# Kernel tuning notes

Measured on AMD Instinct MI355X. Metric: run time of the kernel, lower is better.

Reference implementation:

```python
import jax, jax.numpy as jnp
import numpy as np

B = 1024

def _back_mask(mask_out, selh, selw, s, k, hin, win):
    # Mark which input positions (of this conv) are touched by sampled k x k patches.
    hc, wc = hin - k + 1, win - k + 1
    m = np.zeros((hin, win), np.float32)
    ho, wo = mask_out.shape
    for i in range(ho):
        for j in range(wo):
            if mask_out[i, j] > 0:
                ph = min(i * s + int(selh[i, j]), hc - 1)
                pw = min(j * s + int(selw[i, j]), wc - 1)
                m[ph:ph + k, pw:pw + k] = 1.0
    return m


def setup_inputs() -> dict:
    key = jax.random.key(0)
    ks = jax.random.split(key, 10)
    rng = np.random.default_rng(1)
    # stochastic pooling offsets, top-down as in the torch forward
    selh3 = rng.integers(0, 4, (1, 1)).astype(np.int32)
    selw3 = rng.integers(0, 4, (1, 1)).astype(np.int32)
    mask3 = np.ones((1, 1), np.float32)
    mask2 = _back_mask(mask3, selh3, selw3, s=4, k=3, hin=6, win=6)
    selh2 = rng.integers(0, 2, (6, 6)).astype(np.int32)
    selw2 = rng.integers(0, 2, (6, 6)).astype(np.int32)
    mask1 = _back_mask(mask2, selh2, selw2, s=2, k=3, hin=14, win=14)
    selh1 = rng.integers(0, 2, (14, 14)).astype(np.int32)
    selw1 = rng.integers(0, 2, (14, 14)).astype(np.int32)
    sc = 0.05
    return {
        "x": jax.random.normal(ks[0], (B, 3, 32, 32), jnp.float32),
        "W1": jax.random.normal(ks[1], (200, 3, 5, 5), jnp.float32) * sc,
        "b1": jax.random.normal(ks[2], (200,), jnp.float32) * sc,
        "W2": jax.random.normal(ks[3], (400, 200, 3, 3), jnp.float32) * sc,
        "b2": jax.random.normal(ks[4], (400,), jnp.float32) * sc,
        "W3": jax.random.normal(ks[5], (800, 400, 3, 3), jnp.float32) * sc,
        "b3": jax.random.normal(ks[6], (800,), jnp.float32) * sc,
        "fc_w": jax.random.normal(ks[7], (10, 800), jnp.float32) * sc,
        "fc_b": jax.random.normal(ks[8], (10,), jnp.float32) * sc,
        "selh1": jnp.asarray(selh1), "selw1": jnp.asarray(selw1),
        "selh2": jnp.asarray(selh2), "selw2": jnp.asarray(selw2),
        "selh3": jnp.asarray(selh3), "selw3": jnp.asarray(selw3),
        "mask1": jnp.asarray(mask1), "mask2": jnp.asarray(mask2),
        "mask3": jnp.asarray(mask3),
    }


def _sconv_avg(x, W, b, selh, selw, mask, k, s):
    # Stochastic conv+avgpool: compute stride-1 conv only at one sampled location
    # per pooling window, zero at masked-out output positions.
    Bq, C, H, Wd = x.shape
    hc, wc = H - k + 1, Wd - k + 1
    ho, wo = selh.shape
    ph = jnp.minimum(jnp.arange(ho)[:, None] * s + selh, hc - 1)  # (ho,wo)
    pw = jnp.minimum(jnp.arange(wo)[None, :] * s + selw, wc - 1)
    rows = ph[:, :, :, None] if False else (ph[..., None] + jnp.arange(k))  # (ho,wo,k)
    cols = pw[..., None] + jnp.arange(k)                                    # (ho,wo,k)
    # gather sampled k x k patches -> (B,C,ho,wo,k,k)
    patch = x[:, :, rows[:, :, :, None], cols[:, :, None, :]]
    out = jnp.einsum('bcxyij,ocij->boxy', patch, W) + b[None, :, None, None]
    return out * mask[None, None, :, :]


def reference(x, W1, b1, W2, b2, W3, b3, fc_w, fc_b,
              selh1, selw1, selh2, selw2, selh3, selw3,
              mask1, mask2, mask3):
    h = jax.nn.relu(_sconv_avg(x, W1, b1, selh1, selw1, mask1, k=5, s=2))   # (B,200,14,14)
    h = jax.nn.relu(_sconv_avg(h, W2, b2, selh2, selw2, mask2, k=3, s=2))   # (B,400,6,6)
    h = jax.nn.relu(_sconv_avg(h, W3, b3, selh3, selw3, mask3, k=3, s=4))   # (B,800,1,1)
    h = h.reshape(h.shape[0], -1)                                           # (B,800)
    return h @ fc_w.T + fc_b
```

## Files before the change

kernel.cpp:

```cpp
#include <hip/hip_runtime.h>


#define H1B_OFF 0ULL
#define P2_OFF  80281600ULL
#define W2B_OFF 114491392ULL
#define P3_OFF  116154368ULL
#define W3B_OFF 123625472ULL
#define H3_OFF  129695744ULL
#define W1T_OFF 132972544ULL

typedef unsigned short u16;
typedef short bf16x8 __attribute__((ext_vector_type(8)));
typedef float f32x4 __attribute__((ext_vector_type(4)));

__device__ __forceinline__ u16 f2bf(float f) {
    union { float f; unsigned int u; } v; v.f = f;
    unsigned int u = v.u + 0x7FFFu + ((v.u >> 16) & 1u);
    return (u16)(u >> 16);
}

__global__ __launch_bounds__(256) void wprep(
    const float* __restrict__ W1, const float* __restrict__ W2, const float* __restrict__ W3,
    float* __restrict__ W1t, u16* __restrict__ W2b, u16* __restrict__ W3b)
{
    int idx = blockIdx.x * 256 + threadIdx.x;
    if (idx < 16000) {
        int kk = idx / 200, oc = idx % 200;
        W1t[idx] = (kk < 75) ? W1[oc * 75 + kk] : 0.0f;
    } else if (idx < 16000 + 831488) {
        int j = idx - 16000;
        int oc = j / 1856, kk = j % 1856;
        float v = 0.0f;
        if (oc < 400 && kk < 1800) {
            int k3 = kk / 200, c = kk % 200;
            v = W2[oc * 1800 + c * 9 + k3];
        }
        W2b[j] = f2bf(v);
    } else if (idx < 16000 + 831488 + 3035136) {
        int j = idx - 16000 - 831488;
        int oc = j / 3648, kk = j % 3648;
        float v = 0.0f;
        if (oc < 800 && kk < 3600) {
            int k3 = kk / 400, c = kk % 400;
            v = W3[oc * 3600 + c * 9 + k3];
        }
        W3b[j] = f2bf(v);
    }
}

__global__ __launch_bounds__(256) void l1_kernel(
    const float* __restrict__ x, const float* __restrict__ W1t, const float* __restrict__ b1,
    const int* __restrict__ selh, const int* __restrict__ selw, const float* __restrict__ mask,
    u16* __restrict__ h1b)
{
    const int pos = blockIdx.x;
    const float m = mask[pos];
    if (m == 0.0f) return;
    const int i = pos / 14, j = pos % 14;
    const int b0 = blockIdx.y * 8;
    const int tid = threadIdx.x;
    const int ph = min(i * 2 + selh[pos], 27);
    const int pw = min(j * 2 + selw[pos], 27);

    __shared__ __align__(16) float sm[8 * 80];
    for (int e = tid; e < 640; e += 256) {
        int u = e / 80, kk = e % 80;
        float v = 0.0f;
        if (kk < 75) {
            int c = kk / 25, d = kk % 25;
            v = x[((b0 + u) * 3 + c) * 1024 + (ph + d / 5) * 32 + (pw + d % 5)];
        }
        sm[e] = v;
    }
    __syncthreads();
    if (tid < 200) {
        const int oc = tid;
        float bias = b1[oc];
        float acc[8];
#pragma unroll
        for (int u = 0; u < 8; ++u) acc[u] = bias;
        const float4* sm4 = reinterpret_cast<const float4*>(sm);
        for (int q = 0; q < 20; ++q) {
            float w0 = W1t[(q * 4 + 0) * 200 + oc];
            float w1 = W1t[(q * 4 + 1) * 200 + oc];
            float w2 = W1t[(q * 4 + 2) * 200 + oc];
            float w3 = W1t[(q * 4 + 3) * 200 + oc];
#pragma unroll
            for (int u = 0; u < 8; ++u) {
                float4 p = sm4[u * 20 + q];
                acc[u] = fmaf(w0, p.x, acc[u]);
                acc[u] = fmaf(w1, p.y, acc[u]);
                acc[u] = fmaf(w2, p.z, acc[u]);
                acc[u] = fmaf(w3, p.w, acc[u]);
            }
        }
#pragma unroll
        for (int u = 0; u < 8; ++u)
            h1b[((b0 + u) * 196 + pos) * 200 + oc] = f2bf(fmaxf(acc[u] * m, 0.0f));
    }
}

__global__ __launch_bounds__(256) void im2col2(
    const u16* __restrict__ h1b, const int* __restrict__ selh2, const int* __restrict__ selw2,
    const int* __restrict__ selh3, const int* __restrict__ selw3, u16* __restrict__ P2)
{
    int idx = blockIdx.x * 256 + threadIdx.x;
    int row = idx / 232, ch = idx % 232;
    if (row >= 9216) return;
    int b = row / 9, pidx = row % 9;
    int ph2 = min(selh3[0], 3), pw2 = min(selw3[0], 3);
    int pos = (ph2 + pidx / 3) * 6 + (pw2 + pidx % 3);
    int i = pos / 6, j = pos % 6;
    int ph = min(2 * i + selh2[pos], 11);
    int pw = min(2 * j + selw2[pos], 11);
    uint4 v = {0u, 0u, 0u, 0u};
    if (ch < 225) {
        int k3 = ch / 25, c8 = ch % 25;
        int srow = b * 196 + (ph + k3 / 3) * 14 + (pw + k3 % 3);
        v = *reinterpret_cast<const uint4*>(h1b + srow * 200 + c8 * 8);
    }
    *reinterpret_cast<uint4*>(P2 + (size_t)row * 1856 + ch * 8) = v;
}

__global__ __launch_bounds__(256) void padzero3(u16* __restrict__ P3)
{
    int idx = blockIdx.x * 256 + threadIdx.x;
    if (idx >= 6144) return;
    int b = idx / 6, c = idx % 6;
    uint4 z = {0u, 0u, 0u, 0u};
    *reinterpret_cast<uint4*>(P3 + (size_t)b * 3648 + 3600 + c * 8) = z;
}

__global__ __launch_bounds__(256) void gemm_l2(
    const u16* __restrict__ A, const u16* __restrict__ B,
    const float* __restrict__ bias, u16* __restrict__ P3)
{
    const int KP = 1856, NKT = 29;
    const int m0 = blockIdx.x * 64, n0 = blockIdx.y * 64;
    const int tid = threadIdx.x;
    const int lane = tid & 63, wid = tid >> 6;
    const int wm = wid >> 1, wn = wid & 1;

    __shared__ u16 Asm[64][72];
    __shared__ u16 Bsm[64][72];

    f32x4 zero = {0.f, 0.f, 0.f, 0.f};
    f32x4 acc00 = zero, acc01 = zero, acc10 = zero, acc11 = zero;

    const int ar = tid >> 3, ac = tid & 7;
    const uint4* Ag0 = reinterpret_cast<const uint4*>(A + (size_t)(m0 + ar) * KP + ac * 8);
    const uint4* Ag1 = reinterpret_cast<const uint4*>(A + (size_t)(m0 + ar + 32) * KP + ac * 8);
    const uint4* Bg0 = reinterpret_cast<const uint4*>(B + (size_t)(n0 + ar) * KP + ac * 8);
    const uint4* Bg1 = reinterpret_cast<const uint4*>(B + (size_t)(n0 + ar + 32) * KP + ac * 8);
    uint4* As0 = reinterpret_cast<uint4*>(&Asm[ar][ac * 8]);
    uint4* As1 = reinterpret_cast<uint4*>(&Asm[ar + 32][ac * 8]);
    uint4* Bs0 = reinterpret_cast<uint4*>(&Bsm[ar][ac * 8]);
    uint4* Bs1 = reinterpret_cast<uint4*>(&Bsm[ar + 32][ac * 8]);

    uint4 ra0 = Ag0[0], ra1 = Ag1[0], rb0 = Bg0[0], rb1 = Bg1[0];
    const int r = lane & 15, ks = lane >> 4;
    for (int kt = 0; kt < NKT; ++kt) {
        __syncthreads();
        *As0 = ra0; *As1 = ra1; *Bs0 = rb0; *Bs1 = rb1;
        __syncthreads();
        if (kt + 1 < NKT) {
            ra0 = Ag0[(kt + 1) * 8]; ra1 = Ag1[(kt + 1) * 8];
            rb0 = Bg0[(kt + 1) * 8]; rb1 = Bg1[(kt + 1) * 8];
        }
#pragma unroll
        for (int s = 0; s < 2; ++s) {
            bf16x8 a0 = *reinterpret_cast<const bf16x8*>(&Asm[wm * 32 + r][s * 32 + ks * 8]);
            bf16x8 a1 = *reinterpret_cast<const bf16x8*>(&Asm[wm * 32 + 16 + r][s * 32 + ks * 8]);
            bf16x8 b0 = *reinterpret_cast<const bf16x8*>(&Bsm[wn * 32 + r][s * 32 + ks * 8]);
            bf16x8 b1 = *reinterpret_cast<const bf16x8*>(&Bsm[wn * 32 + 16 + r][s * 32 + ks * 8]);
            acc00 = __builtin_amdgcn_mfma_f32_16x16x32_bf16(a0, b0, acc00, 0, 0, 0);
            acc01 = __builtin_amdgcn_mfma_f32_16x16x32_bf16(a0, b1, acc01, 0, 0, 0);
            acc10 = __builtin_amdgcn_mfma_f32_16x16x32_bf16(a1, b0, acc10, 0, 0, 0);
            acc11 = __builtin_amdgcn_mfma_f32_16x16x32_bf16(a1, b1, acc11, 0, 0, 0);
        }
    }
    const int colb = n0 + wn * 32 + (lane & 15);
    const int rowb = m0 + wm * 32 + ((lane >> 4) << 2);
#define L2STORE(ACC, MR, NR) { \
    int oc = colb + (NR) * 16; \
    if (oc < 400) { float bv = bias[oc]; \
        _Pragma("unroll") \
        for (int rr = 0; rr < 4; ++rr) { \
            int row = rowb + (MR) * 16 + rr; \
            int bq = row / 9, pq = row % 9; \
            P3[(size_t)bq * 3648 + pq * 400 + oc] = f2bf(fmaxf(ACC[rr] + bv, 0.0f)); \
        } } }
    L2STORE(acc00, 0, 0) L2STORE(acc01, 0, 1) L2STORE(acc10, 1, 0) L2STORE(acc11, 1, 1)
#undef L2STORE
}

__global__ __launch_bounds__(256) void gemm_l3(
    const u16* __restrict__ A, const u16* __restrict__ B,
    const float* __restrict__ bias, float* __restrict__ h3)
{
    const int KP = 3648, NKT = 57;
    const int m0 = blockIdx.x * 64, n0 = blockIdx.y * 64;
    const int tid = threadIdx.x;
    const int lane = tid & 63, wid = tid >> 6;
    const int wm = wid >> 1, wn = wid & 1;

    __shared__ u16 Asm[64][72];
    __shared__ u16 Bsm[64][72];

    f32x4 zero = {0.f, 0.f, 0.f, 0.f};
    f32x4 acc00 = zero, acc01 = zero, acc10 = zero, acc11 = zero;

    const int ar = tid >> 3, ac = tid & 7;
    const uint4* Ag0 = reinterpret_cast<const uint4*>(A + (size_t)(m0 + ar) * KP + ac * 8);
    const uint4* Ag1 = reinterpret_cast<const uint4*>(A + (size_t)(m0 + ar + 32) * KP + ac * 8);
    const uint4* Bg0 = reinterpret_cast<const uint4*>(B + (size_t)(n0 + ar) * KP + ac * 8);
    const uint4* Bg1 = reinterpret_cast<const uint4*>(B + (size_t)(n0 + ar + 32) * KP + ac * 8);
    uint4* As0 = reinterpret_cast<uint4*>(&Asm[ar][ac * 8]);
    uint4* As1 = reinterpret_cast<uint4*>(&Asm[ar + 32][ac * 8]);
    uint4* Bs0 = reinterpret_cast<uint4*>(&Bsm[ar][ac * 8]);
    uint4* Bs1 = reinterpret_cast<uint4*>(&Bsm[ar + 32][ac * 8]);

    uint4 ra0 = Ag0[0], ra1 = Ag1[0], rb0 = Bg0[0], rb1 = Bg1[0];
    const int r = lane & 15, ks = lane >> 4;
    for (int kt = 0; kt < NKT; ++kt) {
        __syncthreads();
        *As0 = ra0; *As1 = ra1; *Bs0 = rb0; *Bs1 = rb1;
        __syncthreads();
        if (kt + 1 < NKT) {
            ra0 = Ag0[(kt + 1) * 8]; ra1 = Ag1[(kt + 1) * 8];
            rb0 = Bg0[(kt + 1) * 8]; rb1 = Bg1[(kt + 1) * 8];
        }
#pragma unroll
        for (int s = 0; s < 2; ++s) {
            bf16x8 a0 = *reinterpret_cast<const bf16x8*>(&Asm[wm * 32 + r][s * 32 + ks * 8]);
            bf16x8 a1 = *reinterpret_cast<const bf16x8*>(&Asm[wm * 32 + 16 + r][s * 32 + ks * 8]);
            bf16x8 b0 = *reinterpret_cast<const bf16x8*>(&Bsm[wn * 32 + r][s * 32 + ks * 8]);
            bf16x8 b1 = *reinterpret_cast<const bf16x8*>(&Bsm[wn * 32 + 16 + r][s * 32 + ks * 8]);
            acc00 = __builtin_amdgcn_mfma_f32_16x16x32_bf16(a0, b0, acc00, 0, 0, 0);
            acc01 = __builtin_amdgcn_mfma_f32_16x16x32_bf16(a0, b1, acc01, 0, 0, 0);
            acc10 = __builtin_amdgcn_mfma_f32_16x16x32_bf16(a1, b0, acc10, 0, 0, 0);
            acc11 = __builtin_amdgcn_mfma_f32_16x16x32_bf16(a1, b1, acc11, 0, 0, 0);
        }
    }
    const int colb = n0 + wn * 32 + (lane & 15);
    const int rowb = m0 + wm * 32 + ((lane >> 4) << 2);
#define L3STORE(ACC, MR, NR) { \
    int oc = colb + (NR) * 16; \
    if (oc < 800) { float bv = bias[oc]; \
        _Pragma("unroll") \
        for (int rr = 0; rr < 4; ++rr) { \
            int row = rowb + (MR) * 16 + rr; \
            h3[(size_t)row * 800 + oc] = fmaxf(ACC[rr] + bv, 0.0f); \
        } } }
    L3STORE(acc00, 0, 0) L3STORE(acc01, 0, 1) L3STORE(acc10, 1, 0) L3STORE(acc11, 1, 1)
#undef L3STORE
}

__global__ __launch_bounds__(256) void fc_kernel(
    const float* __restrict__ h3, const float* __restrict__ fcw, const float* __restrict__ fcb,
    float* __restrict__ out)
{
    const int idx = blockIdx.x * 256 + threadIdx.x;
    if (idx >= 1024 * 10) return;
    const int b = idx / 10, o = idx % 10;
    float acc = fcb[o];
    const float4* hp = reinterpret_cast<const float4*>(h3 + b * 800);
    const float4* wp = reinterpret_cast<const float4*>(fcw + o * 800);
    for (int k = 0; k < 200; ++k) {
        float4 h = hp[k], w = wp[k];
        acc = fmaf(h.x, w.x, acc);
        acc = fmaf(h.y, w.y, acc);
        acc = fmaf(h.z, w.z, acc);
        acc = fmaf(h.w, w.w, acc);
    }
    out[idx] = acc;
}

extern "C" void kernel_launch(void* const* d_in, const int* in_sizes, int n_in,
                              void* d_out, int out_size, void* d_ws, size_t ws_size,
                              hipStream_t stream) {
    const float* x     = (const float*)d_in[0];
    const float* W1    = (const float*)d_in[1];
    const float* b1    = (const float*)d_in[2];
    const float* W2    = (const float*)d_in[3];
    const float* b2    = (const float*)d_in[4];
    const float* W3    = (const float*)d_in[5];
    const float* b3    = (const float*)d_in[6];
    const float* fc_w  = (const float*)d_in[7];
    const float* fc_b  = (const float*)d_in[8];
    const int*   selh1 = (const int*)d_in[9];
    const int*   selw1 = (const int*)d_in[10];
    const int*   selh2 = (const int*)d_in[11];
    const int*   selw2 = (const int*)d_in[12];
    const int*   selh3 = (const int*)d_in[13];
    const int*   selw3 = (const int*)d_in[14];
    const float* mask1 = (const float*)d_in[15];

    char* wsb = (char*)d_ws;
    u16*   h1b = (u16*)(wsb + H1B_OFF);
    u16*   P2  = (u16*)(wsb + P2_OFF);
    u16*   W2b = (u16*)(wsb + W2B_OFF);
    u16*   P3  = (u16*)(wsb + P3_OFF);
    u16*   W3b = (u16*)(wsb + W3B_OFF);
    float* h3  = (float*)(wsb + H3_OFF);
    float* W1t = (float*)(wsb + W1T_OFF);
    float* out = (float*)d_out;

    wprep<<<15167, 256, 0, stream>>>(W1, W2, W3, W1t, W2b, W3b);
    l1_kernel<<<dim3(196, 128), 256, 0, stream>>>(x, W1t, b1, selh1, selw1, mask1, h1b);
    im2col2<<<8352, 256, 0, stream>>>(h1b, selh2, selw2, selh3, selw3, P2);
    gemm_l2<<<dim3(144, 7), 256, 0, stream>>>(P2, W2b, b2, P3);
    padzero3<<<24, 256, 0, stream>>>(P3);
    gemm_l3<<<dim3(16, 13), 256, 0, stream>>>(P3, W3b, b3, h3);
    fc_kernel<<<40, 256, 0, stream>>>(h3, fc_w, fc_b, out);
}
```

Baseline: 280.8 us.

## Move layer-1 conv to split-bf16 MFMA GEMM and fuse im2col into GEMM loads

Replaces the scalar FP32 layer-1 kernel with an MFMA bf16 GEMM. Inputs and weights are split into hi/lo bf16 parts (three K segments: hi*hi, lo*hi, hi*lo) to keep near-fp32 accuracy. The separate im2col2 and padzero3 kernels are removed: gemm_l2 now gathers patches directly from h1b, and gemm_l3 zero-fills the padded K region itself. This drops the P2 buffer round trip and two launches, at the cost of more index arithmetic inside the GEMM load path and the extra split-precision multiplies in layer 1.

```diff
diff --git a/kernel.cpp b/kernel.cpp
--- a/kernel.cpp
+++ b/kernel.cpp
@@ -2,12 +2,11 @@
 
 
 #define H1B_OFF 0ULL
-#define P2_OFF  80281600ULL
-#define W2B_OFF 114491392ULL
-#define P3_OFF  116154368ULL
-#define W3B_OFF 123625472ULL
-#define H3_OFF  129695744ULL
-#define W1T_OFF 132972544ULL
+#define W2B_OFF 80281600ULL
+#define P3_OFF  81944576ULL
+#define W3B_OFF 89415680ULL
+#define H3_OFF  95485952ULL
+#define W1S_OFF 98762752ULL
 
 typedef unsigned short u16;
 typedef short bf16x8 __attribute__((ext_vector_type(8)));
@@ -18,17 +17,35 @@
     unsigned int u = v.u + 0x7FFFu + ((v.u >> 16) & 1u);
     return (u16)(u >> 16);
 }
+__device__ __forceinline__ float bf2f(u16 h) {
+    union { unsigned int u; float f; } t; t.u = ((unsigned int)h) << 16;
+    return t.f;
+}
+__device__ __forceinline__ u16 bf_part(float f, int lo) {
+    u16 h = f2bf(f);
+    if (!lo) return h;
+    return f2bf(f - bf2f(h));
+}
 
 __global__ __launch_bounds__(256) void wprep(
     const float* __restrict__ W1, const float* __restrict__ W2, const float* __restrict__ W3,
-    float* __restrict__ W1t, u16* __restrict__ W2b, u16* __restrict__ W3b)
+    u16* __restrict__ W1s, u16* __restrict__ W2b, u16* __restrict__ W3b)
 {
     int idx = blockIdx.x * 256 + threadIdx.x;
-    if (idx < 16000) {
-        int kk = idx / 200, oc = idx % 200;
-        W1t[idx] = (kk < 75) ? W1[oc * 75 + kk] : 0.0f;
-    } else if (idx < 16000 + 831488) {
-        int j = idx - 16000;
+    if (idx < 98304) {
+        int oc = idx / 384, kk = idx % 384;
+        u16 v = 0;
+        if (oc < 200 && kk < 360) {
+            int r3 = kk / 120, d = kk % 120;
+            int c = d / 40, dd = d % 40, di = dd / 8, dj = dd % 8;
+            if (dj < 5) {
+                float w = W1[oc * 75 + c * 25 + di * 5 + dj];
+                v = bf_part(w, r3 == 2);
+            }
+        }
+        W1s[idx] = v;
+    } else if (idx < 98304 + 831488) {
+        int j = idx - 98304;
         int oc = j / 1856, kk = j % 1856;
         float v = 0.0f;
         if (oc < 400 && kk < 1800) {
@@ -36,8 +53,8 @@
             v = W2[oc * 1800 + c * 9 + k3];
         }
         W2b[j] = f2bf(v);
-    } else if (idx < 16000 + 831488 + 3035136) {
-        int j = idx - 16000 - 831488;
+    } else if (idx < 98304 + 831488 + 3035136) {
+        int j = idx - 98304 - 831488;
         int oc = j / 3648, kk = j % 3648;
         float v = 0.0f;
         if (oc < 800 && kk < 3600) {
@@ -48,98 +65,21 @@
     }
 }
 
-__global__ __launch_bounds__(256) void l1_kernel(
-    const float* __restrict__ x, const float* __restrict__ W1t, const float* __restrict__ b1,
+__global__ __launch_bounds__(256) void gemm_l1(
+    const float* __restrict__ x, const u16* __restrict__ W1s, const float* __restrict__ b1,
     const int* __restrict__ selh, const int* __restrict__ selw, const float* __restrict__ mask,
     u16* __restrict__ h1b)
 {
     const int pos = blockIdx.x;
-    const float m = mask[pos];
-    if (m == 0.0f) return;
-    const int i = pos / 14, j = pos % 14;
-    const int b0 = blockIdx.y * 8;
-    const int tid = threadIdx.x;
-    const int ph = min(i * 2 + selh[pos], 27);
-    const int pw = min(j * 2 + selw[pos], 27);
-
-    __shared__ __align__(16) float sm[8 * 80];
-    for (int e = tid; e < 640; e += 256) {
-        int u = e / 80, kk = e % 80;
-        float v = 0.0f;
-        if (kk < 75) {
-            int c = kk / 25, d = kk % 25;
-            v = x[((b0 + u) * 3 + c) * 1024 + (ph + d / 5) * 32 + (pw + d % 5)];
-        }
-        sm[e] = v;
-    }
-    __syncthreads();
-    if (tid < 200) {
-        const int oc = tid;
-        float bias = b1[oc];
-        float acc[8];
-#pragma unroll
-        for (int u = 0; u < 8; ++u) acc[u] = bias;
-        const float4* sm4 = reinterpret_cast<const float4*>(sm);
-        for (int q = 0; q < 20; ++q) {
-            float w0 = W1t[(q * 4 + 0) * 200 + oc];
-            float w1 = W1t[(q * 4 + 1) * 200 + oc];
-            float w2 = W1t[(q * 4 + 2) * 200 + oc];
-            float w3 = W1t[(q * 4 + 3) * 200 + oc];
-#pragma unroll
-            for (int u = 0; u < 8; ++u) {
-                float4 p = sm4[u * 20 + q];
-                acc[u] = fmaf(w0, p.x, acc[u]);
-                acc[u] = fmaf(w1, p.y, acc[u]);
-                acc[u] = fmaf(w2, p.z, acc[u]);
-                acc[u] = fmaf(w3, p.w, acc[u]);
-            }
-        }
-#pragma unroll
-        for (int u = 0; u < 8; ++u)
-            h1b[((b0 + u) * 196 + pos) * 200 + oc] = f2bf(fmaxf(acc[u] * m, 0.0f));
-    }
-}
-
-__global__ __launch_bounds__(256) void im2col2(
-    const u16* __restrict__ h1b, const int* __restrict__ selh2, const int* __restrict__ selw2,
-    const int* __restrict__ selh3, const int* __restrict__ selw3, u16* __restrict__ P2)
-{
-    int idx = blockIdx.x * 256 + threadIdx.x;
-    int row = idx / 232, ch = idx % 232;
-    if (row >= 9216) return;
-    int b = row / 9, pidx = row % 9;
-    int ph2 = min(selh3[0], 3), pw2 = min(selw3[0], 3);
-    int pos = (ph2 + pidx / 3) * 6 + (pw2 + pidx % 3);
-    int i = pos / 6, j = pos % 6;
-    int ph = min(2 * i + selh2[pos], 11);
-    int pw = min(2 * j + selw2[pos], 11);
-    uint4 v = {0u, 0u, 0u, 0u};
-    if (ch < 225) {
-        int k3 = ch / 25, c8 = ch % 25;
-        int srow = b * 196 + (ph + k3 / 3) * 14 + (pw + k3 % 3);
-        v = *reinterpret_cast<const uint4*>(h1b + srow * 200 + c8 * 8);
-    }
-    *reinterpret_cast<uint4*>(P2 + (size_t)row * 1856 + ch * 8) = v;
-}
-
-__global__ __launch_bounds__(256) void padzero3(u16* __restrict__ P3)
-{
-    int idx = blockIdx.x * 256 + threadIdx.x;
-    if (idx >= 6144) return;
-    int b = idx / 6, c = idx % 6;
-    uint4 z = {0u, 0u, 0u, 0u};
-    *reinterpret_cast<uint4*>(P3 + (size_t)b * 3648 + 3600 + c * 8) = z;
-}
-
-__global__ __launch_bounds__(256) void gemm_l2(
-    const u16* __restrict__ A, const u16* __restrict__ B,
-    const float* __restrict__ bias, u16* __restrict__ P3)
-{
-    const int KP = 1856, NKT = 29;
-    const int m0 = blockIdx.x * 64, n0 = blockIdx.y * 64;
+    if (mask[pos] == 0.0f) return;
+    const int NKT = 6, KP = 384;
+    const int b0 = blockIdx.y * 64, n0 = blockIdx.z * 64;
     const int tid = threadIdx.x;
     const int lane = tid & 63, wid = tid >> 6;
     const int wm = wid >> 1, wn = wid & 1;
+    const int i = pos / 14, j = pos % 14;
+    const int ph = min(i * 2 + selh[pos], 27);
+    const int pw = min(j * 2 + selw[pos], 27);
 
     __shared__ u16 Asm[64][72];
     __shared__ u16 Bsm[64][72];
@@ -148,24 +88,38 @@
     f32x4 acc00 = zero, acc01 = zero, acc10 = zero, acc11 = zero;
 
     const int ar = tid >> 3, ac = tid & 7;
-    const uint4* Ag0 = reinterpret_cast<const uint4*>(A + (size_t)(m0 + ar) * KP + ac * 8);
-    const uint4* Ag1 = reinterpret_cast<const uint4*>(A + (size_t)(m0 + ar + 32) * KP + ac * 8);
-    const uint4* Bg0 = reinterpret_cast<const uint4*>(B + (size_t)(n0 + ar) * KP + ac * 8);
-    const uint4* Bg1 = reinterpret_cast<const uint4*>(B + (size_t)(n0 + ar + 32) * KP + ac * 8);
+    auto gatherA = [&](int kt, int r) -> uint4 {
+        int chunk = kt * 8 + ac;
+        int r3 = chunk / 15;
+        union { uint4 v; u16 s[8]; } u;
+        u.v = make_uint4(0u, 0u, 0u, 0u);
+        if (r3 < 3) {
+            int dc = chunk - r3 * 15;
+            int c = dc / 5, di = dc - c * 5;
+            int lo = (r3 == 1);
+            const float* sp = x + (size_t)((b0 + r) * 3 + c) * 1024 + (ph + di) * 32 + pw;
+#pragma unroll
+            for (int t = 0; t < 5; ++t) u.s[t] = bf_part(sp[t], lo);
+        }
+        return u.v;
+    };
+    const uint4* Bg0 = reinterpret_cast<const uint4*>(W1s + (size_t)(n0 + ar) * KP + ac * 8);
+    const uint4* Bg1 = reinterpret_cast<const uint4*>(W1s + (size_t)(n0 + ar + 32) * KP + ac * 8);
     uint4* As0 = reinterpret_cast<uint4*>(&Asm[ar][ac * 8]);
     uint4* As1 = reinterpret_cast<uint4*>(&Asm[ar + 32][ac * 8]);
     uint4* Bs0 = reinterpret_cast<uint4*>(&Bsm[ar][ac * 8]);
     uint4* Bs1 = reinterpret_cast<uint4*>(&Bsm[ar + 32][ac * 8]);
 
-    uint4 ra0 = Ag0[0], ra1 = Ag1[0], rb0 = Bg0[0], rb1 = Bg1[0];
+    uint4 ra0 = gatherA(0, ar), ra1 = gatherA(0, ar + 32);
+    uint4 rb0 = Bg0[0], rb1 = Bg1[0];
     const int r = lane & 15, ks = lane >> 4;
     for (int kt = 0; kt < NKT; ++kt) {
         __syncthreads();
         *As0 = ra0; *As1 = ra1; *Bs0 = rb0; *Bs1 = rb1;
         __syncthreads();
         if (kt + 1 < NKT) {
-            ra0 = Ag0[(kt + 1) * 8]; ra1 = Ag1[(kt + 1) * 8];
-            rb0 = Bg0[(kt + 1) * 8]; rb1 = Bg1[(kt + 1) * 8];
+            ra0 = gatherA(kt + 1, ar); ra1 = gatherA(kt + 1, ar + 32);
+            rb0 = Bg0[(kt + 1) * 8];   rb1 = Bg1[(kt + 1) * 8];
         }
 #pragma unroll
         for (int s = 0; s < 2; ++s) {
@@ -180,6 +134,86 @@
         }
     }
     const int colb = n0 + wn * 32 + (lane & 15);
+    const int rowb = wm * 32 + ((lane >> 4) << 2);
+#define L1STORE(ACC, MR, NR) { \
+    int oc = colb + (NR) * 16; \
+    if (oc < 200) { float bv = b1[oc]; \
+        _Pragma("unroll") \
+        for (int rr = 0; rr < 4; ++rr) { \
+            int b = b0 + rowb + (MR) * 16 + rr; \
+            h1b[((size_t)b * 196 + pos) * 200 + oc] = f2bf(fmaxf(ACC[rr] + bv, 0.0f)); \
+        } } }
+    L1STORE(acc00, 0, 0) L1STORE(acc01, 0, 1) L1STORE(acc10, 1, 0) L1STORE(acc11, 1, 1)
+#undef L1STORE
+}
+
+__global__ __launch_bounds__(256) void gemm_l2(
+    const u16* __restrict__ h1b, const u16* __restrict__ B, const float* __restrict__ bias,
+    const int* __restrict__ selh2, const int* __restrict__ selw2,
+    const int* __restrict__ selh3, const int* __restrict__ selw3,
+    u16* __restrict__ P3)
+{
+    const int KP = 1856, NKT = 29;
+    const int m0 = blockIdx.x * 64, n0 = blockIdx.y * 64;
+    const int tid = threadIdx.x;
+    const int lane = tid & 63, wid = tid >> 6;
+    const int wm = wid >> 1, wn = wid & 1;
+
+    __shared__ u16 Asm[64][72];
+    __shared__ u16 Bsm[64][72];
+
+    f32x4 zero = {0.f, 0.f, 0.f, 0.f};
+    f32x4 acc00 = zero, acc01 = zero, acc10 = zero, acc11 = zero;
+
+    const int ar = tid >> 3, ac = tid & 7;
+    const int ph2 = min(selh3[0], 3), pw2 = min(selw3[0], 3);
+    int mr0 = m0 + ar, mr1 = mr0 + 32;
+    int bq0 = mr0 / 9, p0 = mr0 - bq0 * 9;
+    int bq1 = mr1 / 9, p1 = mr1 - bq1 * 9;
+    int pos0 = (ph2 + p0 / 3) * 6 + (pw2 + p0 % 3);
+    int pos1 = (ph2 + p1 / 3) * 6 + (pw2 + p1 % 3);
+    int base0 = bq0 * 196 + min(2 * (pos0 / 6) + selh2[pos0], 11) * 14
+                          + min(2 * (pos0 % 6) + selw2[pos0], 11);
+    int base1 = bq1 * 196 + min(2 * (pos1 / 6) + selh2[pos1], 11) * 14
+                          + min(2 * (pos1 % 6) + selw2[pos1], 11);
+    auto gatherA = [&](int kt, int base) -> uint4 {
+        int chunk = kt * 8 + ac;
+        if (chunk >= 225) return make_uint4(0u, 0u, 0u, 0u);
+        int k3 = chunk / 25, c8 = chunk - k3 * 25;
+        int srow = base + (k3 / 3) * 14 + (k3 - (k3 / 3) * 3);
+        return *reinterpret_cast<const uint4*>(h1b + (size_t)srow * 200 + c8 * 8);
+    };
+    const uint4* Bg0 = reinterpret_cast<const uint4*>(B + (size_t)(n0 + ar) * KP + ac * 8);
+    const uint4* Bg1 = reinterpret_cast<const uint4*>(B + (size_t)(n0 + ar + 32) * KP + ac * 8);
+    uint4* As0 = reinterpret_cast<uint4*>(&Asm[ar][ac * 8]);
+    uint4* As1 = reinterpret_cast<uint4*>(&Asm[ar + 32][ac * 8]);
+    uint4* Bs0 = reinterpret_cast<uint4*>(&Bsm[ar][ac * 8]);
+    uint4* Bs1 = reinterpret_cast<uint4*>(&Bsm[ar + 32][ac * 8]);
+
+    uint4 ra0 = gatherA(0, base0), ra1 = gatherA(0, base1);
+    uint4 rb0 = Bg0[0], rb1 = Bg1[0];
+    const int r = lane & 15, ks = lane >> 4;
+    for (int kt = 0; kt < NKT; ++kt) {
+        __syncthreads();
+        *As0 = ra0; *As1 = ra1; *Bs0 = rb0; *Bs1 = rb1;
+        __syncthreads();
+        if (kt + 1 < NKT) {
+            ra0 = gatherA(kt + 1, base0); ra1 = gatherA(kt + 1, base1);
+            rb0 = Bg0[(kt + 1) * 8];      rb1 = Bg1[(kt + 1) * 8];
+        }
+#pragma unroll
+        for (int s = 0; s < 2; ++s) {
+            bf16x8 a0 = *reinterpret_cast<const bf16x8*>(&Asm[wm * 32 + r][s * 32 + ks * 8]);
+            bf16x8 a1 = *reinterpret_cast<const bf16x8*>(&Asm[wm * 32 + 16 + r][s * 32 + ks * 8]);
+            bf16x8 b0 = *reinterpret_cast<const bf16x8*>(&Bsm[wn * 32 + r][s * 32 + ks * 8]);
+            bf16x8 b1 = *reinterpret_cast<const bf16x8*>(&Bsm[wn * 32 + 16 + r][s * 32 + ks * 8]);
+            acc00 = __builtin_amdgcn_mfma_f32_16x16x32_bf16(a0, b0, acc00, 0, 0, 0);
+            acc01 = __builtin_amdgcn_mfma_f32_16x16x32_bf16(a0, b1, acc01, 0, 0, 0);
+            acc10 = __builtin_amdgcn_mfma_f32_16x16x32_bf16(a1, b0, acc10, 0, 0, 0);
+            acc11 = __builtin_amdgcn_mfma_f32_16x16x32_bf16(a1, b1, acc11, 0, 0, 0);
+        }
+    }
+    const int colb = n0 + wn * 32 + (lane & 15);
     const int rowb = m0 + wm * 32 + ((lane >> 4) << 2);
 #define L2STORE(ACC, MR, NR) { \
     int oc = colb + (NR) * 16; \
@@ -187,7 +221,7 @@
         _Pragma("unroll") \
         for (int rr = 0; rr < 4; ++rr) { \
             int row = rowb + (MR) * 16 + rr; \
-            int bq = row / 9, pq = row % 9; \
+            int bq = row / 9, pq = row - (row / 9) * 9; \
             P3[(size_t)bq * 3648 + pq * 400 + oc] = f2bf(fmaxf(ACC[rr] + bv, 0.0f)); \
         } } }
     L2STORE(acc00, 0, 0) L2STORE(acc01, 0, 1) L2STORE(acc10, 1, 0) L2STORE(acc11, 1, 1)
@@ -211,8 +245,11 @@
     f32x4 acc00 = zero, acc01 = zero, acc10 = zero, acc11 = zero;
 
     const int ar = tid >> 3, ac = tid & 7;
-    const uint4* Ag0 = reinterpret_cast<const uint4*>(A + (size_t)(m0 + ar) * KP + ac * 8);
-    const uint4* Ag1 = reinterpret_cast<const uint4*>(A + (size_t)(m0 + ar + 32) * KP + ac * 8);
+    auto gatherA = [&](int kt, int row) -> uint4 {
+        int chunk = kt * 8 + ac;
+        if (chunk >= 450) return make_uint4(0u, 0u, 0u, 0u);
+        return *reinterpret_cast<const uint4*>(A + (size_t)row * KP + chunk * 8);
+    };
     const uint4* Bg0 = reinterpret_cast<const uint4*>(B + (size_t)(n0 + ar) * KP + ac * 8);
     const uint4* Bg1 = reinterpret_cast<const uint4*>(B + (size_t)(n0 + ar + 32) * KP + ac * 8);
     uint4* As0 = reinterpret_cast<uint4*>(&Asm[ar][ac * 8]);
@@ -220,15 +257,16 @@
     uint4* Bs0 = reinterpret_cast<uint4*>(&Bsm[ar][ac * 8]);
     uint4* Bs1 = reinterpret_cast<uint4*>(&Bsm[ar + 32][ac * 8]);
 
-    uint4 ra0 = Ag0[0], ra1 = Ag1[0], rb0 = Bg0[0], rb1 = Bg1[0];
+    uint4 ra0 = gatherA(0, m0 + ar), ra1 = gatherA(0, m0 + ar + 32);
+    uint4 rb0 = Bg0[0], rb1 = Bg1[0];
     const int r = lane & 15, ks = lane >> 4;
     for (int kt = 0; kt < NKT; ++kt) {
         __syncthreads();
         *As0 = ra0; *As1 = ra1; *Bs0 = rb0; *Bs1 = rb1;
         __syncthreads();
         if (kt + 1 < NKT) {
-            ra0 = Ag0[(kt + 1) * 8]; ra1 = Ag1[(kt + 1) * 8];
-            rb0 = Bg0[(kt + 1) * 8]; rb1 = Bg1[(kt + 1) * 8];
+            ra0 = gatherA(kt + 1, m0 + ar); ra1 = gatherA(kt + 1, m0 + ar + 32);
+            rb0 = Bg0[(kt + 1) * 8];        rb1 = Bg1[(kt + 1) * 8];
         }
 #pragma unroll
         for (int s = 0; s < 2; ++s) {
@@ -298,19 +336,16 @@
 
     char* wsb = (char*)d_ws;
     u16*   h1b = (u16*)(wsb + H1B_OFF);
-    u16*   P2  = (u16*)(wsb + P2_OFF);
     u16*   W2b = (u16*)(wsb + W2B_OFF);
     u16*   P3  = (u16*)(wsb + P3_OFF);
     u16*   W3b = (u16*)(wsb + W3B_OFF);
     float* h3  = (float*)(wsb + H3_OFF);
-    float* W1t = (float*)(wsb + W1T_OFF);
+    u16*   W1s = (u16*)(wsb + W1S_OFF);
     float* out = (float*)d_out;
 
-    wprep<<<15167, 256, 0, stream>>>(W1, W2, W3, W1t, W2b, W3b);
-    l1_kernel<<<dim3(196, 128), 256, 0, stream>>>(x, W1t, b1, selh1, selw1, mask1, h1b);
-    im2col2<<<8352, 256, 0, stream>>>(h1b, selh2, selw2, selh3, selw3, P2);
-    gemm_l2<<<dim3(144, 7), 256, 0, stream>>>(P2, W2b, b2, P3);
-    padzero3<<<24, 256, 0, stream>>>(P3);
+    wprep<<<15488, 256, 0, stream>>>(W1, W2, W3, W1s, W2b, W3b);
+    gemm_l1<<<dim3(196, 16, 4), 256, 0, stream>>>(x, W1s, b1, selh1, selw1, mask1, h1b);
+    gemm_l2<<<dim3(144, 7), 256, 0, stream>>>(h1b, W2b, b2, selh2, selw2, selh3, selw3, P3);
     gemm_l3<<<dim3(16, 13), 256, 0, stream>>>(P3, W3b, b3, h3);
     fc_kernel<<<40, 256, 0, stream>>>(h3, fc_w, fc_b, out);
 }
```

Result: slower. 366.4 us (+30.5%).
